# Kernel tuning notes

Measured on AMD Instinct MI355X. Metric: run time of the kernel, lower is better.

The kernel has to match this reference:

```python
import jax, jax.numpy as jnp
import numpy as np

DIM, INNER, NH = 256, 64, 8
HD = INNER // NH  # 8
B, H, W = 2, 48, 48
EPS = 1e-6


def _ln2d(x, w, b):
    # channel-first LayerNorm over dim=1, biased variance (matches LayerNorm2d)
    u = x.mean(axis=1, keepdims=True)
    s = ((x - u) ** 2).mean(axis=1, keepdims=True)
    xn = (x - u) / jnp.sqrt(s + EPS)
    return w[None, :, None, None] * xn + b[None, :, None, None]


def _conv1x1(x, w, b):
    return jnp.einsum('oc,bchw->bohw', w, x) + b[None, :, None, None]


def _attn(q, k, v):
    # q,k,v: [B, INNER, H, W] -> global attention over HW tokens per head
    Bq, C, Hh, Ww = q.shape
    split = lambda t: t.reshape(Bq, NH, HD, Hh * Ww)
    q, k, v = split(q), split(k), split(v)
    scale = HD ** -0.5
    attn = jnp.einsum('bhdn,bhdm->bhnm', q, k) * scale  # [B,nh,HW,HW]
    attn = jax.nn.softmax(attn, axis=-1)
    out = jnp.einsum('bhnm,bhdm->bhdn', attn, v)
    return out.reshape(Bq, C, Hh, Ww)


def setup_inputs() -> dict:
    key = jax.random.key(0)
    ks = jax.random.split(key, 12)
    w = lambda k, o, i: jax.random.normal(k, (o, i), dtype=jnp.float32) * 0.02
    d = {
        'f_rgb': jax.random.normal(ks[0], (B, DIM, H, W), dtype=jnp.float32),
        'f_ir': jax.random.normal(ks[1], (B, DIM, H, W), dtype=jnp.float32),
        'nr_w': jnp.ones(DIM), 'nr_b': jnp.zeros(DIM),
        'ni_w': jnp.ones(DIM), 'ni_b': jnp.zeros(DIM),
        'qr_w': w(ks[2], INNER, DIM), 'qr_b': jnp.zeros(INNER),
        'kvi_w': w(ks[3], 2 * INNER, DIM), 'kvi_b': jnp.zeros(2 * INNER),
        'qi_w': w(ks[4], INNER, DIM), 'qi_b': jnp.zeros(INNER),
        'kvr_w': w(ks[5], 2 * INNER, DIM), 'kvr_b': jnp.zeros(2 * INNER),
        'pr_w': w(ks[6], DIM, INNER), 'pr_b': jnp.zeros(DIM),
        'pr_lnw': jnp.ones(DIM), 'pr_lnb': jnp.zeros(DIM),
        'pi_w': w(ks[7], DIM, INNER), 'pi_b': jnp.zeros(DIM),
        'pi_lnw': jnp.ones(DIM), 'pi_lnb': jnp.zeros(DIM),
        'gr_w': w(ks[8], DIM, 2 * DIM), 'gr_b': jnp.zeros(DIM),
        'gi_w': w(ks[9], DIM, 2 * DIM), 'gi_b': jnp.zeros(DIM),
    }
    return d


def reference(f_rgb, f_ir, nr_w, nr_b, ni_w, ni_b, qr_w, qr_b, kvi_w, kvi_b,
              qi_w, qi_b, kvr_w, kvr_b, pr_w, pr_b, pr_lnw, pr_lnb,
              pi_w, pi_b, pi_lnw, pi_lnb, gr_w, gr_b, gi_w, gi_b):
    n_rgb = _ln2d(f_rgb, nr_w, nr_b)
    n_ir = _ln2d(f_ir, ni_w, ni_b)

    # RGB queries attend to IR keys/values
    q_r = _conv1x1(n_rgb, qr_w, qr_b)
    kv_i = _conv1x1(n_ir, kvi_w, kvi_b)
    k_i, v_i = kv_i[:, :INNER], kv_i[:, INNER:]
    rgb_cross = _attn(q_r, k_i, v_i)
    rgb_cross = _ln2d(_conv1x1(rgb_cross, pr_w, pr_b), pr_lnw, pr_lnb)
    gate_r = jax.nn.sigmoid(_conv1x1(jnp.concatenate([f_rgb, rgb_cross], axis=1), gr_w, gr_b))
    f_rgb_out = f_rgb + gate_r * rgb_cross

    # IR queries attend to RGB keys/values
    q_i = _conv1x1(n_ir, qi_w, qi_b)
    kv_r = _conv1x1(n_rgb, kvr_w, kvr_b)
    k_r, v_r = kv_r[:, :INNER], kv_r[:, INNER:]
    ir_cross = _attn(q_i, k_r, v_r)
    ir_cross = _ln2d(_conv1x1(ir_cross, pi_w, pi_b), pi_lnw, pi_lnb)
    gate_i = jax.nn.sigmoid(_conv1x1(jnp.concatenate([f_ir, ir_cross], axis=1), gi_w, gi_b))
    f_ir_out = f_ir + gate_i * ir_cross

    return (f_rgb_out, f_ir_out)
```

## Files before the change

### kernel.cpp

```cpp
#include <hip/hip_runtime.h>

static constexpr int kDim   = 256;
static constexpr int kInner = 64;
static constexpr int kNH    = 8;
static constexpr int kB     = 2;
static constexpr int kP     = 2304;
static constexpr float kScale = 0.35355339059327373f;
static constexpr float kEps   = 1e-6f;

typedef _Float16 half4f __attribute__((ext_vector_type(4)));
typedef _Float16 half8  __attribute__((ext_vector_type(8)));
typedef float    f32x4  __attribute__((ext_vector_type(4)));

static constexpr size_t oXq  = 0;
static constexpr size_t oQ16 = 2359296;
static constexpr size_t oK16 = 2949120;
static constexpr size_t oV16 = 3538944;
static constexpr size_t oA16 = 4128768;
static constexpr size_t oC16 = 4718592;
static constexpr size_t oW16 = 7077888;
static constexpr size_t kInpStride = 294912;

__global__ __launch_bounds__(256) void wcast(
    const float* __restrict__ qr_w, const float* __restrict__ kvr_w,
    const float* __restrict__ qi_w, const float* __restrict__ kvi_w,
    const float* __restrict__ pr_w, const float* __restrict__ pi_w,
    const float* __restrict__ gr_w, const float* __restrict__ gi_w,
    _Float16* __restrict__ w16)
{
    const float* src; _Float16* dst; int n;
    _Float16* Aq = w16;
    _Float16* Ap = w16 + 98304;
    _Float16* Ag = w16 + 131072;
    switch (blockIdx.y) {
        case 0: src = qr_w;  dst = Aq;          n = 16384;  break;
        case 1: src = kvr_w; dst = Aq + 16384;  n = 32768;  break;
        case 2: src = qi_w;  dst = Aq + 49152;  n = 16384;  break;
        case 3: src = kvi_w; dst = Aq + 65536;  n = 32768;  break;
        case 4: src = pr_w;  dst = Ap;          n = 16384;  break;
        case 5: src = pi_w;  dst = Ap + 16384;  n = 16384;  break;
        case 6: src = gr_w;  dst = Ag;          n = 131072; break;
        default:src = gi_w;  dst = Ag + 131072; n = 131072; break;
    }
    for (int i = blockIdx.x * 256 + threadIdx.x; i < n; i += 64 * 256)
        dst[i] = (_Float16)src[i];
}

__global__ __launch_bounds__(256) void ln_pre(
    const float* __restrict__ x0, const float* __restrict__ w0,
    const float* __restrict__ b0, const float* __restrict__ x1,
    const float* __restrict__ w1, const float* __restrict__ b1,
    _Float16* __restrict__ Xq)
{
    __shared__ float sb[16][16];
    __shared__ float ssb[16][16];
    const int fid = blockIdx.x;
    const int xcd = fid & 7, q = fid >> 3;
    const int inp = (xcd >> 2) & 1, bb = (xcd >> 1) & 1, half = xcd & 1;
    const float* x = inp ? x1 : x0;
    const float* w = inp ? w1 : w0;
    const float* b = inp ? b1 : b0;
    const int pos = threadIdx.x & 15;
    const int grp = threadIdx.x >> 4;
    const int p   = half * 1152 + q * 16 + pos;
    const size_t base = (size_t)bb * kDim * kP + p;
    const int c0 = grp * 16;

    float v[16];
    float s = 0.f, ss = 0.f;
    #pragma unroll
    for (int j = 0; j < 16; ++j) {
        v[j] = x[base + (size_t)(c0 + j) * kP];
        s += v[j]; ss += v[j] * v[j];
    }
    sb[grp][pos] = s; ssb[grp][pos] = ss;
    __syncthreads();
    float st = 0.f, sst = 0.f;
    #pragma unroll
    for (int g = 0; g < 16; ++g) { st += sb[g][pos]; sst += ssb[g][pos]; }
    const float mean = st * (1.f / kDim);
    const float rstd = rsqrtf(sst * (1.f / kDim) - mean * mean + kEps);
    half8 h0, h1;
    #pragma unroll
    for (int j = 0; j < 8; ++j) {
        h0[j] = (_Float16)((v[j]     - mean) * rstd * w[c0 + j]     + b[c0 + j]);
        h1[j] = (_Float16)((v[j + 8] - mean) * rstd * w[c0 + j + 8] + b[c0 + j + 8]);
    }
    _Float16* dst = Xq + ((size_t)(inp * 2 + bb) * kP + p) * 256 + c0;
    *(half8*)dst       = h0;
    *(half8*)(dst + 8) = h1;
}

__global__ __launch_bounds__(256) void ln_post(
    const _Float16* __restrict__ c16,
    const float* __restrict__ w0, const float* __restrict__ b0,
    const float* __restrict__ w1, const float* __restrict__ b1,
    const float* __restrict__ f0, const float* __restrict__ f1,
    _Float16* __restrict__ Xg)
{
    __shared__ float sb[16][16];
    __shared__ float ssb[16][16];
    const int fid = blockIdx.x;
    const int xcd = fid & 7, q = fid >> 3;
    const int s = (xcd >> 2) & 1, bb = (xcd >> 1) & 1, half = xcd & 1;
    const float* w = s ? w1 : w0;
    const float* b = s ? b1 : b0;
    const float* F = s ? f1 : f0;
    const int pos = threadIdx.x & 15;
    const int grp = threadIdx.x >> 4;
    const int p   = half * 1152 + q * 16 + pos;
    const int c0  = grp * 16;
    const size_t combo = s * 2 + bb;

    const _Float16* cp = c16 + (combo * kP + p) * 256 + c0;
    const half8 g0 = *(const half8*)cp;
    const half8 g1 = *(const half8*)(cp + 8);
    float v[16];
    float sm = 0.f, ssq = 0.f;
    #pragma unroll
    for (int j = 0; j < 8; ++j) {
        v[j] = (float)g0[j]; v[j + 8] = (float)g1[j];
    }
    #pragma unroll
    for (int j = 0; j < 16; ++j) { sm += v[j]; ssq += v[j] * v[j]; }
    sb[grp][pos] = sm; ssb[grp][pos] = ssq;
    __syncthreads();
    float st = 0.f, sst = 0.f;
    #pragma unroll
    for (int g = 0; g < 16; ++g) { st += sb[g][pos]; sst += ssb[g][pos]; }
    const float mean = st * (1.f / kDim);
    const float rstd = rsqrtf(sst * (1.f / kDim) - mean * mean + kEps);

    _Float16* xrow = Xg + (combo * kP + p) * 512;
    half8 o0, o1;
    #pragma unroll
    for (int j = 0; j < 8; ++j) {
        o0[j] = (_Float16)((v[j]     - mean) * rstd * w[c0 + j]     + b[c0 + j]);
        o1[j] = (_Float16)((v[j + 8] - mean) * rstd * w[c0 + j + 8] + b[c0 + j + 8]);
    }
    *(half8*)(xrow + 256 + c0)     = o0;
    *(half8*)(xrow + 256 + c0 + 8) = o1;
    const size_t fbase = (size_t)bb * kDim * kP + p;
    half8 r0, r1;
    #pragma unroll
    for (int j = 0; j < 8; ++j) {
        r0[j] = (_Float16)F[fbase + (size_t)(c0 + j) * kP];
        r1[j] = (_Float16)F[fbase + (size_t)(c0 + j + 8) * kP];
    }
    *(half8*)(xrow + c0)     = r0;
    *(half8*)(xrow + c0 + 8) = r1;
}

template <int M, int K, int EPI>
__global__ __launch_bounds__(256) void gemm_f16(
    const _Float16* __restrict__ A,
    const _Float16* __restrict__ B,
    const float* __restrict__ b0, const float* __restrict__ b1,
    const float* __restrict__ b2, const float* __restrict__ b3,
    _Float16* __restrict__ o16a, _Float16* __restrict__ o16b, _Float16* __restrict__ o16c,
    const float* __restrict__ f0, const float* __restrict__ f1,
    float* __restrict__ outp)
{
    constexpr int MT64 = M / 64;
    const int fid = blockIdx.x;
    const int xcd = fid & 7, q = fid >> 3;
    const int s = (xcd >> 2) & 1, bb = (xcd >> 1) & 1, half = xcd & 1;
    const int ot64 = (q % MT64) * 64;
    const int pt   = q / MT64;
    const int wv = threadIdx.x >> 6, lane = threadIdx.x & 63;
    const int r16 = lane & 15, g = lane >> 4;
    const int ot = ot64 + wv * 16;
    const int p0 = half * 1152 + pt * 64;
    const int combo = s * 2 + bb;

    const _Float16* Ar = A + ((size_t)s * M + ot + r16) * K + 8 * g;
    const _Float16* Br = B + ((size_t)combo * kP + p0 + r16) * K + 8 * g;
    f32x4 acc0[4], acc1[4];
    #pragma unroll
    for (int ps = 0; ps < 4; ++ps) {
        acc0[ps] = (f32x4){0.f, 0.f, 0.f, 0.f};
        acc1[ps] = (f32x4){0.f, 0.f, 0.f, 0.f};
    }
    #pragma unroll 4
    for (int c0 = 0; c0 < K; c0 += 32) {
        const half8 a8 = *(const half8*)(Ar + c0);
        half8 b8[4];
        #pragma unroll
        for (int ps = 0; ps < 4; ++ps)
            b8[ps] = *(const half8*)(Br + (size_t)(16 * ps) * K + c0);
        const half4f al = {a8[0], a8[1], a8[2], a8[3]};
        const half4f ah = {a8[4], a8[5], a8[6], a8[7]};
        #pragma unroll
        for (int ps = 0; ps < 4; ++ps) {
            const half4f bl = {b8[ps][0], b8[ps][1], b8[ps][2], b8[ps][3]};
            const half4f bh = {b8[ps][4], b8[ps][5], b8[ps][6], b8[ps][7]};
            acc0[ps] = __builtin_amdgcn_mfma_f32_16x16x16f16(al, bl, acc0[ps], 0, 0, 0);
            acc1[ps] = __builtin_amdgcn_mfma_f32_16x16x16f16(ah, bh, acc1[ps], 0, 0, 0);
        }
    }
    const int obase = ot + 4 * g;

    #pragma unroll
    for (int ps = 0; ps < 4; ++ps) {
        float acc[4];
        #pragma unroll
        for (int i = 0; i < 4; ++i) acc[i] = acc0[ps][i] + acc1[ps][i];
        const int p = p0 + 16 * ps + r16;

        if constexpr (EPI == 0) {
            const int dlo = 4 * (g & 1);
            if (ot < 64) {
                const float* qb = s ? b1 : b0;
                const float4 bv = *(const float4*)(qb + obase);
                const int h = (ot >> 3) + (g >> 1);
                half4f o = { (_Float16)((acc[0] + bv.x) * kScale), (_Float16)((acc[1] + bv.y) * kScale),
                             (_Float16)((acc[2] + bv.z) * kScale), (_Float16)((acc[3] + bv.w) * kScale) };
                *(half4f*)(o16a + (((size_t)combo * 8 + h) * kP + p) * 8 + dlo) = o;
            } else if (ot < 128) {
                const float* kb = s ? b3 : b2;
                const float4 bv = *(const float4*)(kb + obase - 64);
                const int h = ((ot - 64) >> 3) + (g >> 1);
                half4f o = { (_Float16)(acc[0] + bv.x), (_Float16)(acc[1] + bv.y),
                             (_Float16)(acc[2] + bv.z), (_Float16)(acc[3] + bv.w) };
                *(half4f*)(o16b + (((size_t)combo * 8 + h) * kP + p) * 8 + dlo) = o;
            } else {
                const float* kb = s ? b3 : b2;
                const float4 bv = *(const float4*)(kb + obase - 64);
                const int h = ((ot - 128) >> 3) + (g >> 1);
                const float* bvp = (const float*)&bv;
                #pragma unroll
                for (int i = 0; i < 4; ++i)
                    o16c[(((size_t)combo * 8 + h) * 8 + dlo + i) * kP + p] = (_Float16)(acc[i] + bvp[i]);
            }
        } else if constexpr (EPI == 1) {
            const float* pb = s ? b1 : b0;
            const float4 bv = *(const float4*)(pb + obase);
            half4f o = { (_Float16)(acc[0] + bv.x), (_Float16)(acc[1] + bv.y),
                         (_Float16)(acc[2] + bv.z), (_Float16)(acc[3] + bv.w) };
            *(half4f*)(o16a + ((size_t)combo * kP + p) * 256 + obase) = o;
        } else {
            const float* gb = s ? b1 : b0;
            const float4 bv = *(const float4*)(gb + obase);
            const float* bvp = (const float*)&bv;
            const half4f cx = *(const half4f*)(B + ((size_t)combo * kP + p) * 512 + 256 + obase);
            const float* F = s ? f1 : f0;
            #pragma unroll
            for (int i = 0; i < 4; ++i) {
                const int o = obase + i;
                const float gt = 1.f / (1.f + __expf(-(acc[i] + bvp[i])));
                const float fb = F[((size_t)bb * kDim + o) * kP + p];
                outp[((size_t)combo * kDim + o) * kP + p] = fb + gt * (float)cx[i];
            }
        }
    }
}

__global__ __launch_bounds__(256) void attn_mfma(
    const _Float16* __restrict__ q16, const _Float16* __restrict__ k16,
    const _Float16* __restrict__ vt16, _Float16* __restrict__ a16)
{
    __shared__ _Float16 Ksm[256 * 24];
    __shared__ _Float16 Vsm[16 * 264];
    const int st = blockIdx.z;
    const _Float16* Qg = q16  + (size_t)st * kInpStride;
    const _Float16* Kg = k16  + (size_t)(1 - st) * kInpStride;
    const _Float16* Vg = vt16 + (size_t)(1 - st) * kInpStride;
    const int bh = blockIdx.y;
    const int bb = bh >> 3, h = bh & 7;
    const int tid  = threadIdx.x;
    const int wv   = tid >> 6;
    const int lane = tid & 63;
    const int r16  = lane & 15;
    const int g    = lane >> 4;

    {
        const float4 z4 = make_float4(0.f, 0.f, 0.f, 0.f);
        *(float4*)(Ksm + tid * 24 + 8) = z4;
        for (int i = tid; i < 264; i += 256)
            *(float4*)(Vsm + 8 * 264 + i * 8) = z4;
    }

    const int qg = blockIdx.x * 64 + wv * 16 + r16;
    half4f qf = (half4f){0, 0, 0, 0};
    if (g < 2) qf = *(const half4f*)(Qg + ((size_t)bh * kP + qg) * 8 + g * 4);

    f32x4 of = (f32x4){0.f, 0.f, 0.f, 0.f};
    float rs = 0.f;

    for (int ch = 0; ch < 9; ++ch) {
        if (ch) __syncthreads();
        const int p0 = ch * 256;
        *(float4*)(Ksm + tid * 24) = *(const float4*)(Kg + ((size_t)bh * kP + p0 + tid) * 8);
        {
            const int d = tid >> 5, c8 = (tid & 31) * 8;
            *(float4*)(Vsm + d * 264 + c8) =
                *(const float4*)(Vg + ((size_t)(bh * 8 + d)) * kP + p0 + c8);
        }
        __syncthreads();
        #pragma unroll
        for (int kt = 0; kt < 16; ++kt) {
            const half4f kf = *(const half4f*)(Ksm + (kt * 16 + r16) * 24 + g * 4);
            f32x4 s = __builtin_amdgcn_mfma_f32_16x16x16f16(kf, qf, (f32x4){0.f,0.f,0.f,0.f}, 0, 0, 0);
            const float e0 = __expf(s[0]), e1 = __expf(s[1]);
            const float e2 = __expf(s[2]), e3 = __expf(s[3]);
            rs += (e0 + e1) + (e2 + e3);
            const half4f pf = { (_Float16)e0, (_Float16)e1, (_Float16)e2, (_Float16)e3 };
            const half4f vf = *(const half4f*)(Vsm + r16 * 264 + kt * 16 + g * 4);
            of = __builtin_amdgcn_mfma_f32_16x16x16f16(vf, pf, of, 0, 0, 0);
        }
    }
    rs += __shfl_xor(rs, 16, 64);
    rs += __shfl_xor(rs, 32, 64);
    const float inv = 1.f / rs;
    if (g < 2) {
        half4f o = { (_Float16)(of[0] * inv), (_Float16)(of[1] * inv),
                     (_Float16)(of[2] * inv), (_Float16)(of[3] * inv) };
        *(half4f*)(a16 + ((size_t)(st * 2 + bb) * kP + qg) * 64 + h * 8 + g * 4) = o;
    }
}

extern "C" void kernel_launch(void* const* d_in, const int* in_sizes, int n_in,
                              void* d_out, int out_size, void* d_ws, size_t ws_size,
                              hipStream_t stream)
{
    const float* f_rgb  = (const float*)d_in[0];
    const float* f_ir   = (const float*)d_in[1];
    const float* nr_w   = (const float*)d_in[2];
    const float* nr_b   = (const float*)d_in[3];
    const float* ni_w   = (const float*)d_in[4];
    const float* ni_b   = (const float*)d_in[5];
    const float* qr_w   = (const float*)d_in[6];
    const float* qr_b   = (const float*)d_in[7];
    const float* kvi_w  = (const float*)d_in[8];
    const float* kvi_b  = (const float*)d_in[9];
    const float* qi_w   = (const float*)d_in[10];
    const float* qi_b   = (const float*)d_in[11];
    const float* kvr_w  = (const float*)d_in[12];
    const float* kvr_b  = (const float*)d_in[13];
    const float* pr_w   = (const float*)d_in[14];
    const float* pr_b   = (const float*)d_in[15];
    const float* pr_lnw = (const float*)d_in[16];
    const float* pr_lnb = (const float*)d_in[17];
    const float* pi_w   = (const float*)d_in[18];
    const float* pi_b   = (const float*)d_in[19];
    const float* pi_lnw = (const float*)d_in[20];
    const float* pi_lnb = (const float*)d_in[21];
    const float* gr_w   = (const float*)d_in[22];
    const float* gr_b   = (const float*)d_in[23];
    const float* gi_w   = (const float*)d_in[24];
    const float* gi_b   = (const float*)d_in[25];

    _Float16* hb   = (_Float16*)d_ws;
    _Float16* Xq   = hb + oXq;
    _Float16* q16  = hb + oQ16;
    _Float16* k16  = hb + oK16;
    _Float16* vt16 = hb + oV16;
    _Float16* a16  = hb + oA16;
    _Float16* Xg   = hb;
    _Float16* c16  = hb + oC16;
    _Float16* W16  = hb + oW16;
    _Float16* Aq   = W16;
    _Float16* Ap   = W16 + 98304;
    _Float16* Ag   = W16 + 131072;

    float* outp = (float*)d_out;
    const dim3 blk(256);

    wcast<<<dim3(64, 8), blk, 0, stream>>>(qr_w, kvr_w, qi_w, kvi_w, pr_w, pi_w, gr_w, gi_w, W16);
    ln_pre<<<dim3(576), blk, 0, stream>>>(f_rgb, nr_w, nr_b, f_ir, ni_w, ni_b, Xq);
    gemm_f16<192, 256, 0><<<dim3(432), blk, 0, stream>>>(
        Aq, Xq, qr_b, qi_b, kvr_b, kvi_b, q16, k16, vt16, nullptr, nullptr, nullptr);
    attn_mfma<<<dim3(36, 16, 2), blk, 0, stream>>>(q16, k16, vt16, a16);
    gemm_f16<256, 64, 1><<<dim3(576), blk, 0, stream>>>(
        Ap, a16, pr_b, pi_b, nullptr, nullptr, c16, nullptr, nullptr, nullptr, nullptr, nullptr);
    ln_post<<<dim3(576), blk, 0, stream>>>(c16, pr_lnw, pr_lnb, pi_lnw, pi_lnb,
                                           f_rgb, f_ir, Xg);
    gemm_f16<256, 512, 2><<<dim3(576), blk, 0, stream>>>(
        Ag, Xg, gr_b, gi_b, nullptr, nullptr, nullptr, nullptr, nullptr, f_rgb, f_ir, outp);
}
```

Baseline: 117.3 us.

## Merge weight cast into LN prep, relayout attention LDS and fold rowsum into MFMA

Fuses the weight-cast kernel into the pre-LayerNorm kernel as extra blocks, removing one launch. In the attention kernel, K and V are stored in LDS in MFMA-fragment order so each lane reads a contiguous half4 with no bank-conflicting stride. A row of ones is placed in the padded V rows so the softmax denominator comes out of the PV MFMA itself, which removes the per-step scalar adds and the cross-lane reductions. The exp-to-fp16 conversion now uses packed round-toward-zero conversions, which slightly changes rounding.

```diff
diff --git a/kernel.cpp b/kernel.cpp
--- a/kernel.cpp
+++ b/kernel.cpp
@@ -8,6 +8,7 @@
 static constexpr float kScale = 0.35355339059327373f;
 static constexpr float kEps   = 1e-6f;
 
+typedef __fp16   fp16x2 __attribute__((ext_vector_type(2)));
 typedef _Float16 half4f __attribute__((ext_vector_type(4)));
 typedef _Float16 half8  __attribute__((ext_vector_type(8)));
 typedef float    f32x4  __attribute__((ext_vector_type(4)));
@@ -21,37 +22,38 @@
 static constexpr size_t oW16 = 7077888;
 static constexpr size_t kInpStride = 294912;
 
-__global__ __launch_bounds__(256) void wcast(
+__global__ __launch_bounds__(256) void prep(
+    const float* __restrict__ x0, const float* __restrict__ w0,
+    const float* __restrict__ b0, const float* __restrict__ x1,
+    const float* __restrict__ w1, const float* __restrict__ b1,
+    _Float16* __restrict__ Xq,
     const float* __restrict__ qr_w, const float* __restrict__ kvr_w,
     const float* __restrict__ qi_w, const float* __restrict__ kvi_w,
     const float* __restrict__ pr_w, const float* __restrict__ pi_w,
     const float* __restrict__ gr_w, const float* __restrict__ gi_w,
     _Float16* __restrict__ w16)
 {
-    const float* src; _Float16* dst; int n;
-    _Float16* Aq = w16;
-    _Float16* Ap = w16 + 98304;
-    _Float16* Ag = w16 + 131072;
-    switch (blockIdx.y) {
-        case 0: src = qr_w;  dst = Aq;          n = 16384;  break;
-        case 1: src = kvr_w; dst = Aq + 16384;  n = 32768;  break;
-        case 2: src = qi_w;  dst = Aq + 49152;  n = 16384;  break;
-        case 3: src = kvi_w; dst = Aq + 65536;  n = 32768;  break;
-        case 4: src = pr_w;  dst = Ap;          n = 16384;  break;
-        case 5: src = pi_w;  dst = Ap + 16384;  n = 16384;  break;
-        case 6: src = gr_w;  dst = Ag;          n = 131072; break;
-        default:src = gi_w;  dst = Ag + 131072; n = 131072; break;
-    }
-    for (int i = blockIdx.x * 256 + threadIdx.x; i < n; i += 64 * 256)
-        dst[i] = (_Float16)src[i];
-}
-
-__global__ __launch_bounds__(256) void ln_pre(
-    const float* __restrict__ x0, const float* __restrict__ w0,
-    const float* __restrict__ b0, const float* __restrict__ x1,
-    const float* __restrict__ w1, const float* __restrict__ b1,
-    _Float16* __restrict__ Xq)
-{
+    if (blockIdx.x >= 576) {
+        const int flat = blockIdx.x - 576;
+        const int y = flat >> 6, x = flat & 63;
+        const float* src; _Float16* dst; int n;
+        _Float16* Aq = w16;
+        _Float16* Ap = w16 + 98304;
+        _Float16* Ag = w16 + 131072;
+        switch (y) {
+            case 0: src = qr_w;  dst = Aq;          n = 16384;  break;
+            case 1: src = kvr_w; dst = Aq + 16384;  n = 32768;  break;
+            case 2: src = qi_w;  dst = Aq + 49152;  n = 16384;  break;
+            case 3: src = kvi_w; dst = Aq + 65536;  n = 32768;  break;
+            case 4: src = pr_w;  dst = Ap;          n = 16384;  break;
+            case 5: src = pi_w;  dst = Ap + 16384;  n = 16384;  break;
+            case 6: src = gr_w;  dst = Ag;          n = 131072; break;
+            default:src = gi_w;  dst = Ag + 131072; n = 131072; break;
+        }
+        for (int i = x * 256 + threadIdx.x; i < n; i += 64 * 256)
+            dst[i] = (_Float16)src[i];
+        return;
+    }
     __shared__ float sb[16][16];
     __shared__ float ssb[16][16];
     const int fid = blockIdx.x;
@@ -259,8 +261,8 @@
     const _Float16* __restrict__ q16, const _Float16* __restrict__ k16,
     const _Float16* __restrict__ vt16, _Float16* __restrict__ a16)
 {
-    __shared__ _Float16 Ksm[256 * 24];
-    __shared__ _Float16 Vsm[16 * 264];
+    __shared__ _Float16 Ksm[16 * 64 * 4];
+    __shared__ _Float16 Vsm[16 * 64 * 4];
     const int st = blockIdx.z;
     const _Float16* Qg = q16  + (size_t)st * kInpStride;
     const _Float16* Kg = k16  + (size_t)(1 - st) * kInpStride;
@@ -273,11 +275,16 @@
     const int r16  = lane & 15;
     const int g    = lane >> 4;
 
-    {
-        const float4 z4 = make_float4(0.f, 0.f, 0.f, 0.f);
-        *(float4*)(Ksm + tid * 24 + 8) = z4;
-        for (int i = tid; i < 264; i += 256)
-            *(float4*)(Vsm + 8 * 264 + i * 8) = z4;
+    #pragma unroll
+    for (int j = 0; j < 2; ++j) {
+        const int s = tid + 256 * j;
+        const int kt = s >> 5, m = s & 31;
+        *(half4f*)(Ksm + (kt * 64 + 32 + m) * 4) = (half4f){0, 0, 0, 0};
+        const int rv = 8 + (m & 7), gv = m >> 3;
+        const half4f vv = (rv == 8)
+            ? (half4f){(_Float16)1.f, (_Float16)1.f, (_Float16)1.f, (_Float16)1.f}
+            : (half4f){0, 0, 0, 0};
+        *(half4f*)(Vsm + (kt * 64 + gv * 16 + rv) * 4) = vv;
     }
 
     const int qg = blockIdx.x * 64 + wv * 16 + r16;
@@ -285,33 +292,41 @@
     if (g < 2) qf = *(const half4f*)(Qg + ((size_t)bh * kP + qg) * 8 + g * 4);
 
     f32x4 of = (f32x4){0.f, 0.f, 0.f, 0.f};
-    float rs = 0.f;
 
     for (int ch = 0; ch < 9; ++ch) {
         if (ch) __syncthreads();
         const int p0 = ch * 256;
-        *(float4*)(Ksm + tid * 24) = *(const float4*)(Kg + ((size_t)bh * kP + p0 + tid) * 8);
+        {
+            const half8 k8 = *(const half8*)(Kg + ((size_t)bh * kP + p0 + tid) * 8);
+            _Float16* base = Ksm + ((tid >> 4) * 64 + (tid & 15)) * 4;
+            *(half4f*)base        = (half4f){k8[0], k8[1], k8[2], k8[3]};
+            *(half4f*)(base + 64) = (half4f){k8[4], k8[5], k8[6], k8[7]};
+        }
         {
             const int d = tid >> 5, c8 = (tid & 31) * 8;
-            *(float4*)(Vsm + d * 264 + c8) =
-                *(const float4*)(Vg + ((size_t)(bh * 8 + d)) * kP + p0 + c8);
+            const half8 v8 = *(const half8*)(Vg + (size_t)(bh * 8 + d) * kP + p0 + c8);
+            const int kt = c8 >> 4, gv = (c8 & 15) >> 2;
+            _Float16* base = Vsm + (kt * 64 + gv * 16 + d) * 4;
+            *(half4f*)base        = (half4f){v8[0], v8[1], v8[2], v8[3]};
+            *(half4f*)(base + 64) = (half4f){v8[4], v8[5], v8[6], v8[7]};
         }
         __syncthreads();
         #pragma unroll
         for (int kt = 0; kt < 16; ++kt) {
-            const half4f kf = *(const half4f*)(Ksm + (kt * 16 + r16) * 24 + g * 4);
-            f32x4 s = __builtin_amdgcn_mfma_f32_16x16x16f16(kf, qf, (f32x4){0.f,0.f,0.f,0.f}, 0, 0, 0);
-            const float e0 = __expf(s[0]), e1 = __expf(s[1]);
-            const float e2 = __expf(s[2]), e3 = __expf(s[3]);
-            rs += (e0 + e1) + (e2 + e3);
-            const half4f pf = { (_Float16)e0, (_Float16)e1, (_Float16)e2, (_Float16)e3 };
-            const half4f vf = *(const half4f*)(Vsm + r16 * 264 + kt * 16 + g * 4);
+            const half4f kf = *(const half4f*)(Ksm + kt * 256 + lane * 4);
+            f32x4 sv = __builtin_amdgcn_mfma_f32_16x16x16f16(kf, qf, (f32x4){0.f,0.f,0.f,0.f}, 0, 0, 0);
+            const float e0 = __expf(sv[0]), e1 = __expf(sv[1]);
+            const float e2 = __expf(sv[2]), e3 = __expf(sv[3]);
+            const fp16x2 lo = __builtin_amdgcn_cvt_pkrtz(e0, e1);
+            const fp16x2 hi = __builtin_amdgcn_cvt_pkrtz(e2, e3);
+            const half4f pf = { (_Float16)lo[0], (_Float16)lo[1],
+                                (_Float16)hi[0], (_Float16)hi[1] };
+            const half4f vf = *(const half4f*)(Vsm + kt * 256 + lane * 4);
             of = __builtin_amdgcn_mfma_f32_16x16x16f16(vf, pf, of, 0, 0, 0);
         }
     }
-    rs += __shfl_xor(rs, 16, 64);
-    rs += __shfl_xor(rs, 32, 64);
-    const float inv = 1.f / rs;
+    const float rsv = __shfl(of[0], 32 + r16, 64);
+    const float inv = 1.f / rsv;
     if (g < 2) {
         half4f o = { (_Float16)(of[0] * inv), (_Float16)(of[1] * inv),
                      (_Float16)(of[2] * inv), (_Float16)(of[3] * inv) };
@@ -366,8 +381,8 @@
     float* outp = (float*)d_out;
     const dim3 blk(256);
 
-    wcast<<<dim3(64, 8), blk, 0, stream>>>(qr_w, kvr_w, qi_w, kvi_w, pr_w, pi_w, gr_w, gi_w, W16);
-    ln_pre<<<dim3(576), blk, 0, stream>>>(f_rgb, nr_w, nr_b, f_ir, ni_w, ni_b, Xq);
+    prep<<<dim3(1088), blk, 0, stream>>>(f_rgb, nr_w, nr_b, f_ir, ni_w, ni_b, Xq,
+                                         qr_w, kvr_w, qi_w, kvi_w, pr_w, pi_w, gr_w, gi_w, W16);
     gemm_f16<192, 256, 0><<<dim3(432), blk, 0, stream>>>(
         Aq, Xq, qr_b, qi_b, kvr_b, kvi_b, q16, k16, vt16, nullptr, nullptr, nullptr);
     attn_mfma<<<dim3(36, 16, 2), blk, 0, stream>>>(q16, k16, vt16, a16);
```

Measured after the change: 111.7 us. -4.8%, faster.
